# Kernel tuning notes

Hardware: AMD Instinct MI355X
Metric: run time of the kernel (lower is better)

Reference implementation:

```python
import jax, jax.numpy as jnp
from jax import lax
import numpy as np

SEQ_LEN, N_FEAT, H, BATCH = 128, 32, 64, 4096


def _lstm_seq(x, W, U, b):
    """Keras-style LSTM with activation=relu, recurrent_activation=sigmoid.
    x: [B,T,F]; W: [F,4H]; U: [H,4H]; b: [4H]. Returns all hidden states [B,T,H]."""
    B = x.shape[0]
    Hd = U.shape[0]
    # precompute input projections for all timesteps (one big GEMM)
    zx = jnp.einsum('btf,fg->btg', x, W) + b  # [B,T,4H]

    def step(carry, zx_t):
        h, c = carry
        z = zx_t + h @ U  # [B,4H]
        i, f, g, o = jnp.split(z, 4, axis=-1)  # Keras gate order i,f,c,o
        i = jax.nn.sigmoid(i)
        f = jax.nn.sigmoid(f)
        o = jax.nn.sigmoid(o)
        g = jax.nn.relu(g)          # activation='relu' on candidate
        c = f * c + i * g
        h = o * jax.nn.relu(c)      # activation='relu' on cell output
        return (h, c), h

    init = (jnp.zeros((B, Hd), x.dtype), jnp.zeros((B, Hd), x.dtype))
    _, hs = lax.scan(step, init, jnp.swapaxes(zx, 0, 1))  # hs: [T,B,H]
    return jnp.swapaxes(hs, 0, 1)


def setup_inputs() -> dict:
    key = jax.random.key(0)
    ks = jax.random.split(key, 7)
    s = lambda fan_in: 1.0 / np.sqrt(fan_in)
    return {
        'x': jax.random.normal(ks[0], (BATCH, SEQ_LEN, N_FEAT), jnp.float32),
        'enc_W': jax.random.normal(ks[1], (N_FEAT, 4 * H), jnp.float32) * s(N_FEAT),
        'enc_U': jax.random.normal(ks[2], (H, 4 * H), jnp.float32) * s(H),
        'enc_b': jnp.zeros((4 * H,), jnp.float32),
        'dec_W': jax.random.normal(ks[3], (H, 4 * H), jnp.float32) * s(H),
        'dec_U': jax.random.normal(ks[4], (H, 4 * H), jnp.float32) * s(H),
        'dec_b': jnp.zeros((4 * H,), jnp.float32),
        'dense_W': jax.random.normal(ks[5], (H, N_FEAT), jnp.float32) * s(H),
        'dense_b': jnp.zeros((N_FEAT,), jnp.float32),
    }


def reference(x, enc_W, enc_U, enc_b, dec_W, dec_U, dec_b, dense_W, dense_b):
    # encoder: LSTM, keep only last hidden state (return_sequences=False)
    enc_hs = _lstm_seq(x, enc_W, enc_U, enc_b)            # [B,T,H]
    encoded = enc_hs[:, -1, :]                            # [B,H]
    # decoder: RepeatVector(T) -> LSTM(return_sequences=True) -> TimeDistributed(Dense)
    rep = jnp.broadcast_to(encoded[:, None, :], (x.shape[0], SEQ_LEN, H))
    dec_hs = _lstm_seq(rep, dec_W, dec_U, dec_b)          # [B,T,H]
    out = jnp.einsum('bth,hf->btf', dec_hs, dense_W) + dense_b  # [B,T,F]
    return out
```

## Files before the change

### kernel.cpp

```cpp
#include <hip/hip_runtime.h>
#include <hip/hip_bf16.h>


typedef __bf16 bf16x8 __attribute__((ext_vector_type(8)));
typedef float f32x4 __attribute__((ext_vector_type(4)));
typedef float f32x8 __attribute__((ext_vector_type(8)));

struct frag3 { bf16x8 p1, p2, p3; };
struct bf3 { __bf16 a, b, c; };

#define NEG_LOG2E (-1.44269504088896340736f)

__device__ __forceinline__ float fast_sig(float z) {
    return __builtin_amdgcn_rcpf(1.0f + __builtin_amdgcn_exp2f(z));
}

__device__ __forceinline__ void hbar() {
    asm volatile("s_waitcnt lgkmcnt(0)\n\ts_barrier" ::: "memory");
}

__device__ __forceinline__ f32x4 mfma6(const frag3& a, const frag3& b, f32x4 c) {
    c = __builtin_amdgcn_mfma_f32_16x16x32_bf16(a.p1, b.p1, c, 0, 0, 0);
    c = __builtin_amdgcn_mfma_f32_16x16x32_bf16(a.p1, b.p2, c, 0, 0, 0);
    c = __builtin_amdgcn_mfma_f32_16x16x32_bf16(a.p2, b.p1, c, 0, 0, 0);
    c = __builtin_amdgcn_mfma_f32_16x16x32_bf16(a.p2, b.p2, c, 0, 0, 0);
    c = __builtin_amdgcn_mfma_f32_16x16x32_bf16(a.p1, b.p3, c, 0, 0, 0);
    c = __builtin_amdgcn_mfma_f32_16x16x32_bf16(a.p3, b.p1, c, 0, 0, 0);
    return c;
}

__device__ __forceinline__ f32x4 mfma3(const frag3& a, const frag3& b, f32x4 c) {
    c = __builtin_amdgcn_mfma_f32_16x16x32_bf16(a.p1, b.p1, c, 0, 0, 0);
    c = __builtin_amdgcn_mfma_f32_16x16x32_bf16(a.p1, b.p2, c, 0, 0, 0);
    c = __builtin_amdgcn_mfma_f32_16x16x32_bf16(a.p2, b.p1, c, 0, 0, 0);
    return c;
}

__device__ __forceinline__ bf3 split3(float v) {
    bf3 r;
    r.a = (__bf16)v;
    float r1 = v - (float)r.a;
    r.b = (__bf16)r1;
    r.c = (__bf16)(r1 - (float)r.b);
    return r;
}

template<int LD>
__device__ __forceinline__ frag3 load_fragB3(const float* __restrict__ M,
                                             int k0, int col, int lq,
                                             float scale) {
    frag3 r;
    const float* p = M + (size_t)(k0 + lq * 8) * LD + col;
#pragma unroll
    for (int e = 0; e < 8; ++e) {
        bf3 s = split3(p[(size_t)e * LD] * scale);
        r.p1[e] = s.a; r.p2[e] = s.b; r.p3[e] = s.c;
    }
    return r;
}

__device__ __forceinline__ frag3 split3_vec(f32x8 v) {
    frag3 r;
#pragma unroll
    for (int e = 0; e < 8; ++e) {
        bf3 s = split3(v[e]);
        r.p1[e] = s.a; r.p2[e] = s.b; r.p3[e] = s.c;
    }
    return r;
}

__device__ __forceinline__ int swz(int row, int byteoff) {
    return row * 128 + (byteoff ^ ((row & 7) << 4));
}

__global__ __launch_bounds__(256, 1)
void lstm_ae_kernel(const float* __restrict__ x,
                    const float* __restrict__ eW, const float* __restrict__ eU,
                    const float* __restrict__ eb,
                    const float* __restrict__ dW, const float* __restrict__ dU,
                    const float* __restrict__ db,
                    const float* __restrict__ nW, const float* __restrict__ nb,
                    float* __restrict__ out)
{
    const int tid = threadIdx.x;
    const int wv  = tid >> 6;
    const int ln  = tid & 63;
    const int l16 = ln & 15;
    const int lq  = ln >> 4;
    const int b0  = blockIdx.x << 4;
    const int wcol = wv * 16 + l16;

    __shared__ __align__(16) unsigned char hraw[2][3][2048];

    int offw[4];
#pragma unroll
    for (int r = 0; r < 4; ++r) offw[r] = swz(lq * 4 + r, wcol * 2);
    const int offr0 = swz(l16, lq * 16);
    const int offr1 = swz(l16, 64 + lq * 16);

    const float gscale[4] = {NEG_LOG2E, NEG_LOG2E, 1.0f, NEG_LOG2E};

    frag3 W3[4], U3[4][2];
    float bz[4];
#pragma unroll
    for (int g = 0; g < 4; ++g) {
        W3[g]    = load_fragB3<256>(eW, 0,  g * 64 + wcol, lq, gscale[g]);
        U3[g][0] = load_fragB3<256>(eU, 0,  g * 64 + wcol, lq, gscale[g]);
        U3[g][1] = load_fragB3<256>(eU, 32, g * 64 + wcol, lq, gscale[g]);
        bz[g]    = eb[g * 64 + wcol] * gscale[g];
    }

    const f32x4 zero4 = {0.f, 0.f, 0.f, 0.f};
    f32x4 cs = zero4;
    frag3 ha0, ha1;
#pragma unroll
    for (int e = 0; e < 8; ++e) {
        ha0.p1[e] = (__bf16)0.f; ha0.p2[e] = (__bf16)0.f; ha0.p3[e] = (__bf16)0.f;
        ha1.p1[e] = (__bf16)0.f; ha1.p2[e] = (__bf16)0.f; ha1.p3[e] = (__bf16)0.f;
    }

    const float* xbase = x + (size_t)(b0 + l16) * (128 * 32) + lq * 8;
    f32x8 xv0 = *(const f32x8*)(xbase);
    f32x8 xv1 = *(const f32x8*)(xbase + 32);

    int q = 0;
#pragma unroll 2
    for (int t = 0; t < 128; ++t) {
        const int tn = (t + 2 < 128) ? (t + 2) : 127;
        f32x8 xv2 = *(const f32x8*)(xbase + (size_t)tn * 32);

        frag3 xa3 = split3_vec(xv0);

        f32x4 a0[4], a1[4], a2[4];
#pragma unroll
        for (int g = 0; g < 4; ++g) {
            f32x4 zb = {bz[g], bz[g], bz[g], bz[g]};
            a0[g] = mfma6(xa3, W3[g],    zb);
            a1[g] = mfma6(ha0, U3[g][0], zero4);
            a2[g] = mfma6(ha1, U3[g][1], zero4);
        }
        f32x4 z[4];
#pragma unroll
        for (int g = 0; g < 4; ++g) z[g] = (a0[g] + a1[g]) + a2[g];
#pragma unroll
        for (int r = 0; r < 4; ++r) {
            float ig = fast_sig(z[0][r]);
            float fg = fast_sig(z[1][r]);
            float gg = fmaxf(z[2][r], 0.f);
            float og = fast_sig(z[3][r]);
            cs[r] = fg * cs[r] + ig * gg;
            float hv = og * fmaxf(cs[r], 0.f);
            bf3 s = split3(hv);
            *(__bf16*)(hraw[q][0] + offw[r]) = s.a;
            *(__bf16*)(hraw[q][1] + offw[r]) = s.b;
            *(__bf16*)(hraw[q][2] + offw[r]) = s.c;
        }
        hbar();
        ha0.p1 = *(const bf16x8*)(hraw[q][0] + offr0);
        ha0.p2 = *(const bf16x8*)(hraw[q][1] + offr0);
        ha0.p3 = *(const bf16x8*)(hraw[q][2] + offr0);
        ha1.p1 = *(const bf16x8*)(hraw[q][0] + offr1);
        ha1.p2 = *(const bf16x8*)(hraw[q][1] + offr1);
        ha1.p3 = *(const bf16x8*)(hraw[q][2] + offr1);
        q ^= 1;
        xv0 = xv1; xv1 = xv2;
    }

    frag3 dU3[4][2];
    f32x4 zx[4];
#pragma unroll
    for (int g = 0; g < 4; ++g) {
        frag3 w0 = load_fragB3<256>(dW, 0,  g * 64 + wcol, lq, gscale[g]);
        frag3 w1 = load_fragB3<256>(dW, 32, g * 64 + wcol, lq, gscale[g]);
        dU3[g][0] = load_fragB3<256>(dU, 0,  g * 64 + wcol, lq, gscale[g]);
        dU3[g][1] = load_fragB3<256>(dU, 32, g * 64 + wcol, lq, gscale[g]);
        float bb = db[g * 64 + wcol] * gscale[g];
        f32x4 zc = {bb, bb, bb, bb};
        zc = mfma6(ha0, w0, zc);
        zc = mfma6(ha1, w1, zc);
        zx[g] = zc;
    }
    frag3 DN3[2];
    float ob = 0.f;
    if (wv < 2) {
        DN3[0] = load_fragB3<32>(nW, 0,  wv * 16 + l16, lq, 1.0f);
        DN3[1] = load_fragB3<32>(nW, 32, wv * 16 + l16, lq, 1.0f);
        ob     = nb[wv * 16 + l16];
    }

#pragma unroll
    for (int e = 0; e < 8; ++e) {
        ha0.p1[e] = (__bf16)0.f; ha0.p2[e] = (__bf16)0.f; ha0.p3[e] = (__bf16)0.f;
        ha1.p1[e] = (__bf16)0.f; ha1.p2[e] = (__bf16)0.f; ha1.p3[e] = (__bf16)0.f;
    }
    cs = zero4;
    q = 0;
#pragma unroll 2
    for (int t = 0; t < 128; ++t) {
        f32x4 a0[4], a1[4];
#pragma unroll
        for (int g = 0; g < 4; ++g) {
            a0[g] = mfma6(ha0, dU3[g][0], zx[g]);
            a1[g] = mfma6(ha1, dU3[g][1], zero4);
        }
        f32x4 z[4];
#pragma unroll
        for (int g = 0; g < 4; ++g) z[g] = a0[g] + a1[g];
#pragma unroll
        for (int r = 0; r < 4; ++r) {
            float ig = fast_sig(z[0][r]);
            float fg = fast_sig(z[1][r]);
            float gg = fmaxf(z[2][r], 0.f);
            float og = fast_sig(z[3][r]);
            cs[r] = fg * cs[r] + ig * gg;
            float hv = og * fmaxf(cs[r], 0.f);
            bf3 s = split3(hv);
            *(__bf16*)(hraw[q][0] + offw[r]) = s.a;
            *(__bf16*)(hraw[q][1] + offw[r]) = s.b;
            *(__bf16*)(hraw[q][2] + offw[r]) = s.c;
        }
        hbar();
        ha0.p1 = *(const bf16x8*)(hraw[q][0] + offr0);
        ha0.p2 = *(const bf16x8*)(hraw[q][1] + offr0);
        ha0.p3 = *(const bf16x8*)(hraw[q][2] + offr0);
        ha1.p1 = *(const bf16x8*)(hraw[q][0] + offr1);
        ha1.p2 = *(const bf16x8*)(hraw[q][1] + offr1);
        ha1.p3 = *(const bf16x8*)(hraw[q][2] + offr1);
        if (wv < 2) {
            f32x4 ob4 = {ob, ob, ob, ob};
            f32x4 d0 = mfma3(ha0, DN3[0], ob4);
            f32x4 d1 = mfma3(ha1, DN3[1], zero4);
            f32x4 oa = d0 + d1;
#pragma unroll
            for (int r = 0; r < 4; ++r)
                out[((size_t)(b0 + lq * 4 + r) * 128 + t) * 32 + wv * 16 + l16] = oa[r];
        }
        q ^= 1;
    }
}

extern "C" void kernel_launch(void* const* d_in, const int* in_sizes, int n_in,
                              void* d_out, int out_size, void* d_ws, size_t ws_size,
                              hipStream_t stream) {
    const float* x  = (const float*)d_in[0];
    const float* eW = (const float*)d_in[1];
    const float* eU = (const float*)d_in[2];
    const float* eb = (const float*)d_in[3];
    const float* dW = (const float*)d_in[4];
    const float* dU = (const float*)d_in[5];
    const float* db = (const float*)d_in[6];
    const float* nW = (const float*)d_in[7];
    const float* nb = (const float*)d_in[8];
    float* out = (float*)d_out;

    hipLaunchKernelGGL(lstm_ae_kernel, dim3(4096 / 16), dim3(256), 0, stream,
                       x, eW, eU, eb, dW, dU, db, nW, nb, out);
}
```

Measured before the change: 257.7 us.

## Split recurrent GEMM K-dimension across two warp groups with LDS partial-sum exchange

Result: no change. 254.9 us (-1.1%).

```diff
diff --git a/kernel.cpp b/kernel.cpp
--- a/kernel.cpp
+++ b/kernel.cpp
@@ -69,11 +69,20 @@
     return r;
 }
 
+__device__ __forceinline__ frag3 zfrag() {
+    frag3 r;
+#pragma unroll
+    for (int e = 0; e < 8; ++e) {
+        r.p1[e] = (__bf16)0.f; r.p2[e] = (__bf16)0.f; r.p3[e] = (__bf16)0.f;
+    }
+    return r;
+}
+
 __device__ __forceinline__ int swz(int row, int byteoff) {
     return row * 128 + (byteoff ^ ((row & 7) << 4));
 }
 
-__global__ __launch_bounds__(256, 1)
+__global__ __launch_bounds__(512, 1)
 void lstm_ae_kernel(const float* __restrict__ x,
                     const float* __restrict__ eW, const float* __restrict__ eU,
                     const float* __restrict__ eb,
@@ -87,155 +96,248 @@
     const int ln  = tid & 63;
     const int l16 = ln & 15;
     const int lq  = ln >> 4;
+    const int pr  = wv & 3;
     const int b0  = blockIdx.x << 4;
-    const int wcol = wv * 16 + l16;
-
-    __shared__ __align__(16) unsigned char hraw[2][3][2048];
-
-    int offw[4];
-#pragma unroll
-    for (int r = 0; r < 4; ++r) offw[r] = swz(lq * 4 + r, wcol * 2);
+    const int wcol = pr * 16 + l16;
+    const int role = __builtin_amdgcn_readfirstlane(tid >> 8);
+    const int roleoff = role * 2;
+
+    __shared__ __align__(16) unsigned char hraw[3][2048];
+    __shared__ float zbuf[4][2][2][4][64];
+
+    int offwr[2];
+#pragma unroll
+    for (int r2 = 0; r2 < 2; ++r2)
+        offwr[r2] = swz(lq * 4 + roleoff + r2, wcol * 2);
     const int offr0 = swz(l16, lq * 16);
     const int offr1 = swz(l16, 64 + lq * 16);
 
     const float gscale[4] = {NEG_LOG2E, NEG_LOG2E, 1.0f, NEG_LOG2E};
-
-    frag3 W3[4], U3[4][2];
-    float bz[4];
-#pragma unroll
-    for (int g = 0; g < 4; ++g) {
-        W3[g]    = load_fragB3<256>(eW, 0,  g * 64 + wcol, lq, gscale[g]);
-        U3[g][0] = load_fragB3<256>(eU, 0,  g * 64 + wcol, lq, gscale[g]);
-        U3[g][1] = load_fragB3<256>(eU, 32, g * 64 + wcol, lq, gscale[g]);
-        bz[g]    = eb[g * 64 + wcol] * gscale[g];
-    }
-
     const f32x4 zero4 = {0.f, 0.f, 0.f, 0.f};
-    f32x4 cs = zero4;
-    frag3 ha0, ha1;
-#pragma unroll
-    for (int e = 0; e < 8; ++e) {
-        ha0.p1[e] = (__bf16)0.f; ha0.p2[e] = (__bf16)0.f; ha0.p3[e] = (__bf16)0.f;
-        ha1.p1[e] = (__bf16)0.f; ha1.p2[e] = (__bf16)0.f; ha1.p3[e] = (__bf16)0.f;
-    }
-
-    const float* xbase = x + (size_t)(b0 + l16) * (128 * 32) + lq * 8;
-    f32x8 xv0 = *(const f32x8*)(xbase);
-    f32x8 xv1 = *(const f32x8*)(xbase + 32);
-
-    int q = 0;
-#pragma unroll 2
-    for (int t = 0; t < 128; ++t) {
-        const int tn = (t + 2 < 128) ? (t + 2) : 127;
-        f32x8 xv2 = *(const f32x8*)(xbase + (size_t)tn * 32);
-
-        frag3 xa3 = split3_vec(xv0);
-
-        f32x4 a0[4], a1[4], a2[4];
+
+    if (role == 0) {
+        frag3 W3[4], U3a[2];
+        float bz[4];
 #pragma unroll
         for (int g = 0; g < 4; ++g) {
-            f32x4 zb = {bz[g], bz[g], bz[g], bz[g]};
-            a0[g] = mfma6(xa3, W3[g],    zb);
-            a1[g] = mfma6(ha0, U3[g][0], zero4);
-            a2[g] = mfma6(ha1, U3[g][1], zero4);
-        }
-        f32x4 z[4];
-#pragma unroll
-        for (int g = 0; g < 4; ++g) z[g] = (a0[g] + a1[g]) + a2[g];
-#pragma unroll
-        for (int r = 0; r < 4; ++r) {
-            float ig = fast_sig(z[0][r]);
-            float fg = fast_sig(z[1][r]);
-            float gg = fmaxf(z[2][r], 0.f);
-            float og = fast_sig(z[3][r]);
-            cs[r] = fg * cs[r] + ig * gg;
-            float hv = og * fmaxf(cs[r], 0.f);
-            bf3 s = split3(hv);
-            *(__bf16*)(hraw[q][0] + offw[r]) = s.a;
-            *(__bf16*)(hraw[q][1] + offw[r]) = s.b;
-            *(__bf16*)(hraw[q][2] + offw[r]) = s.c;
-        }
-        hbar();
-        ha0.p1 = *(const bf16x8*)(hraw[q][0] + offr0);
-        ha0.p2 = *(const bf16x8*)(hraw[q][1] + offr0);
-        ha0.p3 = *(const bf16x8*)(hraw[q][2] + offr0);
-        ha1.p1 = *(const bf16x8*)(hraw[q][0] + offr1);
-        ha1.p2 = *(const bf16x8*)(hraw[q][1] + offr1);
-        ha1.p3 = *(const bf16x8*)(hraw[q][2] + offr1);
-        q ^= 1;
-        xv0 = xv1; xv1 = xv2;
-    }
-
-    frag3 dU3[4][2];
-    f32x4 zx[4];
-#pragma unroll
-    for (int g = 0; g < 4; ++g) {
-        frag3 w0 = load_fragB3<256>(dW, 0,  g * 64 + wcol, lq, gscale[g]);
-        frag3 w1 = load_fragB3<256>(dW, 32, g * 64 + wcol, lq, gscale[g]);
-        dU3[g][0] = load_fragB3<256>(dU, 0,  g * 64 + wcol, lq, gscale[g]);
-        dU3[g][1] = load_fragB3<256>(dU, 32, g * 64 + wcol, lq, gscale[g]);
-        float bb = db[g * 64 + wcol] * gscale[g];
-        f32x4 zc = {bb, bb, bb, bb};
-        zc = mfma6(ha0, w0, zc);
-        zc = mfma6(ha1, w1, zc);
-        zx[g] = zc;
-    }
-    frag3 DN3[2];
-    float ob = 0.f;
-    if (wv < 2) {
-        DN3[0] = load_fragB3<32>(nW, 0,  wv * 16 + l16, lq, 1.0f);
-        DN3[1] = load_fragB3<32>(nW, 32, wv * 16 + l16, lq, 1.0f);
-        ob     = nb[wv * 16 + l16];
-    }
-
-#pragma unroll
-    for (int e = 0; e < 8; ++e) {
-        ha0.p1[e] = (__bf16)0.f; ha0.p2[e] = (__bf16)0.f; ha0.p3[e] = (__bf16)0.f;
-        ha1.p1[e] = (__bf16)0.f; ha1.p2[e] = (__bf16)0.f; ha1.p3[e] = (__bf16)0.f;
-    }
-    cs = zero4;
-    q = 0;
-#pragma unroll 2
-    for (int t = 0; t < 128; ++t) {
-        f32x4 a0[4], a1[4];
+            W3[g] = load_fragB3<256>(eW, 0, g * 64 + wcol, lq, gscale[g]);
+            bz[g] = eb[g * 64 + wcol] * gscale[g];
+        }
+        U3a[0] = load_fragB3<256>(eU, 0, 0 * 64 + wcol, lq, gscale[0]);
+        U3a[1] = load_fragB3<256>(eU, 0, 1 * 64 + wcol, lq, gscale[1]);
+
+        frag3 ha0 = zfrag();
+        float cs2[2] = {0.f, 0.f};
+
+        const float* xbase = x + (size_t)(b0 + l16) * (128 * 32) + lq * 8;
+        f32x8 xv0 = *(const f32x8*)(xbase);
+        f32x8 xv1 = *(const f32x8*)(xbase + 32);
+
+#pragma unroll 1
+        for (int t = 0; t < 128; ++t) {
+            const int tn = (t + 2 < 128) ? (t + 2) : 127;
+            f32x8 xv2 = *(const f32x8*)(xbase + (size_t)tn * 32);
+            frag3 xa3 = split3_vec(xv0);
+
+            f32x4 acc[4];
+#pragma unroll
+            for (int g = 0; g < 4; ++g) {
+                f32x4 a = {bz[g], bz[g], bz[g], bz[g]};
+                acc[g] = mfma6(xa3, W3[g], a);
+            }
+            acc[0] = mfma6(ha0, U3a[0], acc[0]);
+            acc[1] = mfma6(ha0, U3a[1], acc[1]);
+
+#pragma unroll
+            for (int r2 = 0; r2 < 2; ++r2)
+#pragma unroll
+                for (int g = 0; g < 4; ++g)
+                    zbuf[pr][0][r2][g][ln] = acc[g][2 + r2];
+            hbar();
+#pragma unroll
+            for (int r2 = 0; r2 < 2; ++r2) {
+                float zi = acc[0][r2] + zbuf[pr][1][r2][0][ln];
+                float zf = acc[1][r2] + zbuf[pr][1][r2][1][ln];
+                float zg = acc[2][r2] + zbuf[pr][1][r2][2][ln];
+                float zo = acc[3][r2] + zbuf[pr][1][r2][3][ln];
+                float ig = fast_sig(zi), fg = fast_sig(zf), og = fast_sig(zo);
+                float gg = fmaxf(zg, 0.f);
+                cs2[r2] = fg * cs2[r2] + ig * gg;
+                float hv = og * fmaxf(cs2[r2], 0.f);
+                bf3 s = split3(hv);
+                *(__bf16*)(hraw[0] + offwr[r2]) = s.a;
+                *(__bf16*)(hraw[1] + offwr[r2]) = s.b;
+                *(__bf16*)(hraw[2] + offwr[r2]) = s.c;
+            }
+            hbar();
+            ha0.p1 = *(const bf16x8*)(hraw[0] + offr0);
+            ha0.p2 = *(const bf16x8*)(hraw[1] + offr0);
+            ha0.p3 = *(const bf16x8*)(hraw[2] + offr0);
+            xv0 = xv1; xv1 = xv2;
+        }
+
+        frag3 e0, e1;
+        e0.p1 = *(const bf16x8*)(hraw[0] + offr0);
+        e0.p2 = *(const bf16x8*)(hraw[1] + offr0);
+        e0.p3 = *(const bf16x8*)(hraw[2] + offr0);
+        e1.p1 = *(const bf16x8*)(hraw[0] + offr1);
+        e1.p2 = *(const bf16x8*)(hraw[1] + offr1);
+        e1.p3 = *(const bf16x8*)(hraw[2] + offr1);
+        f32x4 zx[4];
+        frag3 dU0[4];
 #pragma unroll
         for (int g = 0; g < 4; ++g) {
-            a0[g] = mfma6(ha0, dU3[g][0], zx[g]);
-            a1[g] = mfma6(ha1, dU3[g][1], zero4);
-        }
-        f32x4 z[4];
-#pragma unroll
-        for (int g = 0; g < 4; ++g) z[g] = a0[g] + a1[g];
-#pragma unroll
-        for (int r = 0; r < 4; ++r) {
-            float ig = fast_sig(z[0][r]);
-            float fg = fast_sig(z[1][r]);
-            float gg = fmaxf(z[2][r], 0.f);
-            float og = fast_sig(z[3][r]);
-            cs[r] = fg * cs[r] + ig * gg;
-            float hv = og * fmaxf(cs[r], 0.f);
-            bf3 s = split3(hv);
-            *(__bf16*)(hraw[q][0] + offw[r]) = s.a;
-            *(__bf16*)(hraw[q][1] + offw[r]) = s.b;
-            *(__bf16*)(hraw[q][2] + offw[r]) = s.c;
-        }
-        hbar();
-        ha0.p1 = *(const bf16x8*)(hraw[q][0] + offr0);
-        ha0.p2 = *(const bf16x8*)(hraw[q][1] + offr0);
-        ha0.p3 = *(const bf16x8*)(hraw[q][2] + offr0);
-        ha1.p1 = *(const bf16x8*)(hraw[q][0] + offr1);
-        ha1.p2 = *(const bf16x8*)(hraw[q][1] + offr1);
-        ha1.p3 = *(const bf16x8*)(hraw[q][2] + offr1);
-        if (wv < 2) {
-            f32x4 ob4 = {ob, ob, ob, ob};
-            f32x4 d0 = mfma3(ha0, DN3[0], ob4);
-            f32x4 d1 = mfma3(ha1, DN3[1], zero4);
-            f32x4 oa = d0 + d1;
-#pragma unroll
-            for (int r = 0; r < 4; ++r)
-                out[((size_t)(b0 + lq * 4 + r) * 128 + t) * 32 + wv * 16 + l16] = oa[r];
-        }
-        q ^= 1;
+            frag3 w0 = load_fragB3<256>(dW, 0,  g * 64 + wcol, lq, gscale[g]);
+            frag3 w1 = load_fragB3<256>(dW, 32, g * 64 + wcol, lq, gscale[g]);
+            float bb = db[g * 64 + wcol] * gscale[g];
+            f32x4 a = {bb, bb, bb, bb};
+            a = mfma6(e0, w0, a);
+            a = mfma6(e1, w1, a);
+            zx[g] = a;
+            dU0[g] = load_fragB3<256>(dU, 0, g * 64 + wcol, lq, gscale[g]);
+        }
+
+        frag3 hd0 = zfrag();
+        cs2[0] = cs2[1] = 0.f;
+#pragma unroll 1
+        for (int t = 0; t < 128; ++t) {
+            f32x4 acc[4];
+#pragma unroll
+            for (int g = 0; g < 4; ++g) acc[g] = mfma6(hd0, dU0[g], zx[g]);
+#pragma unroll
+            for (int r2 = 0; r2 < 2; ++r2)
+#pragma unroll
+                for (int g = 0; g < 4; ++g)
+                    zbuf[pr][0][r2][g][ln] = acc[g][2 + r2];
+            hbar();
+#pragma unroll
+            for (int r2 = 0; r2 < 2; ++r2) {
+                float zi = acc[0][r2] + zbuf[pr][1][r2][0][ln];
+                float zf = acc[1][r2] + zbuf[pr][1][r2][1][ln];
+                float zg = acc[2][r2] + zbuf[pr][1][r2][2][ln];
+                float zo = acc[3][r2] + zbuf[pr][1][r2][3][ln];
+                float ig = fast_sig(zi), fg = fast_sig(zf), og = fast_sig(zo);
+                float gg = fmaxf(zg, 0.f);
+                cs2[r2] = fg * cs2[r2] + ig * gg;
+                float hv = og * fmaxf(cs2[r2], 0.f);
+                bf3 s = split3(hv);
+                *(__bf16*)(hraw[0] + offwr[r2]) = s.a;
+                *(__bf16*)(hraw[1] + offwr[r2]) = s.b;
+                *(__bf16*)(hraw[2] + offwr[r2]) = s.c;
+            }
+            hbar();
+            hd0.p1 = *(const bf16x8*)(hraw[0] + offr0);
+            hd0.p2 = *(const bf16x8*)(hraw[1] + offr0);
+            hd0.p3 = *(const bf16x8*)(hraw[2] + offr0);
+        }
+    } else {
+        frag3 U3b[2], U3c[4];
+        U3b[0] = load_fragB3<256>(eU, 0, 2 * 64 + wcol, lq, gscale[2]);
+        U3b[1] = load_fragB3<256>(eU, 0, 3 * 64 + wcol, lq, gscale[3]);
+#pragma unroll
+        for (int g = 0; g < 4; ++g)
+            U3c[g] = load_fragB3<256>(eU, 32, g * 64 + wcol, lq, gscale[g]);
+
+        frag3 ha0 = zfrag(), ha1 = zfrag();
+        float cs2[2] = {0.f, 0.f};
+
+#pragma unroll 1
+        for (int t = 0; t < 128; ++t) {
+            f32x4 acc[4];
+            acc[0] = mfma6(ha1, U3c[0], zero4);
+            acc[1] = mfma6(ha1, U3c[1], zero4);
+            acc[2] = mfma6(ha0, U3b[0], zero4);
+            acc[2] = mfma6(ha1, U3c[2], acc[2]);
+            acc[3] = mfma6(ha0, U3b[1], zero4);
+            acc[3] = mfma6(ha1, U3c[3], acc[3]);
+
+#pragma unroll
+            for (int r2 = 0; r2 < 2; ++r2)
+#pragma unroll
+                for (int g = 0; g < 4; ++g)
+                    zbuf[pr][1][r2][g][ln] = acc[g][r2];
+            hbar();
+#pragma unroll
+            for (int r2 = 0; r2 < 2; ++r2) {
+                float zi = acc[0][2 + r2] + zbuf[pr][0][r2][0][ln];
+                float zf = acc[1][2 + r2] + zbuf[pr][0][r2][1][ln];
+                float zg = acc[2][2 + r2] + zbuf[pr][0][r2][2][ln];
+                float zo = acc[3][2 + r2] + zbuf[pr][0][r2][3][ln];
+                float ig = fast_sig(zi), fg = fast_sig(zf), og = fast_sig(zo);
+                float gg = fmaxf(zg, 0.f);
+                cs2[r2] = fg * cs2[r2] + ig * gg;
+                float hv = og * fmaxf(cs2[r2], 0.f);
+                bf3 s = split3(hv);
+                *(__bf16*)(hraw[0] + offwr[r2]) = s.a;
+                *(__bf16*)(hraw[1] + offwr[r2]) = s.b;
+                *(__bf16*)(hraw[2] + offwr[r2]) = s.c;
+            }
+            hbar();
+            ha0.p1 = *(const bf16x8*)(hraw[0] + offr0);
+            ha0.p2 = *(const bf16x8*)(hraw[1] + offr0);
+            ha0.p3 = *(const bf16x8*)(hraw[2] + offr0);
+            ha1.p1 = *(const bf16x8*)(hraw[0] + offr1);
+            ha1.p2 = *(const bf16x8*)(hraw[1] + offr1);
+            ha1.p3 = *(const bf16x8*)(hraw[2] + offr1);
+        }
+
+        frag3 dU1[4];
+#pragma unroll
+        for (int g = 0; g < 4; ++g)
+            dU1[g] = load_fragB3<256>(dU, 32, g * 64 + wcol, lq, gscale[g]);
+        const bool dn = (wv < 6);
+        frag3 DN0 = zfrag(), DN1 = zfrag(), hdd = zfrag();
+        float obv = 0.f;
+        if (dn) {
+            DN0 = load_fragB3<32>(nW, 0,  (wv - 4) * 16 + l16, lq, 1.0f);
+            DN1 = load_fragB3<32>(nW, 32, (wv - 4) * 16 + l16, lq, 1.0f);
+            obv = nb[(wv - 4) * 16 + l16];
+        }
+
+        frag3 hd1 = zfrag();
+        cs2[0] = cs2[1] = 0.f;
+#pragma unroll 1
+        for (int t = 0; t < 128; ++t) {
+            f32x4 acc[4];
+#pragma unroll
+            for (int g = 0; g < 4; ++g) acc[g] = mfma6(hd1, dU1[g], zero4);
+#pragma unroll
+            for (int r2 = 0; r2 < 2; ++r2)
+#pragma unroll
+                for (int g = 0; g < 4; ++g)
+                    zbuf[pr][1][r2][g][ln] = acc[g][r2];
+            hbar();
+#pragma unroll
+            for (int r2 = 0; r2 < 2; ++r2) {
+                float zi = acc[0][2 + r2] + zbuf[pr][0][r2][0][ln];
+                float zf = acc[1][2 + r2] + zbuf[pr][0][r2][1][ln];
+                float zg = acc[2][2 + r2] + zbuf[pr][0][r2][2][ln];
+                float zo = acc[3][2 + r2] + zbuf[pr][0][r2][3][ln];
+                float ig = fast_sig(zi), fg = fast_sig(zf), og = fast_sig(zo);
+                float gg = fmaxf(zg, 0.f);
+                cs2[r2] = fg * cs2[r2] + ig * gg;
+                float hv = og * fmaxf(cs2[r2], 0.f);
+                bf3 s = split3(hv);
+                *(__bf16*)(hraw[0] + offwr[r2]) = s.a;
+                *(__bf16*)(hraw[1] + offwr[r2]) = s.b;
+                *(__bf16*)(hraw[2] + offwr[r2]) = s.c;
+            }
+            hbar();
+            hd1.p1 = *(const bf16x8*)(hraw[0] + offr1);
+            hd1.p2 = *(const bf16x8*)(hraw[1] + offr1);
+            hd1.p3 = *(const bf16x8*)(hraw[2] + offr1);
+            if (dn) {
+                hdd.p1 = *(const bf16x8*)(hraw[0] + offr0);
+                hdd.p2 = *(const bf16x8*)(hraw[1] + offr0);
+                f32x4 oa = {obv, obv, obv, obv};
+                oa = mfma3(hdd, DN0, oa);
+                oa = mfma3(hd1, DN1, oa);
+#pragma unroll
+                for (int r = 0; r < 4; ++r)
+                    out[((size_t)(b0 + lq * 4 + r) * 128 + t) * 32
+                        + (wv - 4) * 16 + l16] = oa[r];
+            }
+        }
     }
 }
 
@@ -253,6 +355,6 @@
     const float* nb = (const float*)d_in[8];
     float* out = (float*)d_out;
 
-    hipLaunchKernelGGL(lstm_ae_kernel, dim3(4096 / 16), dim3(256), 0, stream,
+    hipLaunchKernelGGL(lstm_ae_kernel, dim3(4096 / 16), dim3(512), 0, stream,
                        x, eW, eU, eb, dW, dU, db, nW, nb, out);
 }
```
